# Performance work log

Hardware: AMD Instinct MI355X
Metric: run time of the kernel (lower is better)

The kernel has to match this reference:

```python
import jax, jax.numpy as jnp
import numpy as np

B, N, C = 4, 1024, 512
H = 8
HD = C // H
SCALE = HD ** (-0.5)


def setup_inputs() -> dict:
    key = jax.random.key(0)
    ks = jax.random.split(key, 12)
    s = 0.02
    return {
        "x": jax.random.normal(ks[0], (B, N, C), dtype=jnp.float32),
        "y": jax.random.normal(ks[1], (B, N, C), dtype=jnp.float32),
        "Wqkv1": jax.random.normal(ks[2], (4 * C, C), dtype=jnp.float32) * s,
        "Wqkv2": jax.random.normal(ks[3], (4 * C, C), dtype=jnp.float32) * s,
        "W1": jax.random.normal(ks[4], (C, C), dtype=jnp.float32) * s,
        "b1": jnp.zeros((C,), dtype=jnp.float32),
        "W2": jax.random.normal(ks[5], (C, C), dtype=jnp.float32) * s,
        "b2": jnp.zeros((C,), dtype=jnp.float32),
        "W3": jax.random.normal(ks[6], (C, C), dtype=jnp.float32) * s,
        "b3": jnp.zeros((C,), dtype=jnp.float32),
        "W4": jax.random.normal(ks[7], (C, C), dtype=jnp.float32) * s,
        "b4": jnp.zeros((C,), dtype=jnp.float32),
    }


def _l2norm(t, eps=1e-12):
    # matches F.normalize(dim=-1)
    n = jnp.sqrt(jnp.sum(t * t, axis=-1, keepdims=True))
    return t / jnp.maximum(n, eps)


def _ortho_loss(q, qt):
    # q, qt: [B, H, N, HD]
    qn = _l2norm(q)
    qtn = _l2norm(qt)
    prod = jnp.einsum("bhnd,bhmd->bhnm", qn, qtn)  # [B,H,N,N]
    eye = jnp.eye(N, dtype=prod.dtype)
    off = prod * (1.0 - eye)
    # fro-norm squared of off-diagonal, divided by B*N*N (as in source)
    return jnp.sum(off * off) / (B * N * N)


def _qkv(inp, W):
    # inp: [B,N,C], W: [4C, C] -> [4, B, H, N, HD]
    t = (inp @ W.T).reshape(B, N, 4, H, HD)
    return jnp.transpose(t, (2, 0, 3, 1, 4))


def _attn(q, k, v):
    # q,k,v: [B,H,N,HD] -> [B,N,C]
    scores = jnp.einsum("bhnd,bhmd->bhnm", q, k) * SCALE
    a = jax.nn.softmax(scores, axis=-1)
    o = jnp.einsum("bhnm,bhmd->bhnd", a, v)
    return jnp.transpose(o, (0, 2, 1, 3)).reshape(B, N, C)


def reference(x, y, Wqkv1, Wqkv2, W1, b1, W2, b2, W3, b3, W4, b4):
    qkv1 = _qkv(x, Wqkv1)
    qkv2 = _qkv(y, Wqkv2)
    qx, kx, vx, qtx = qkv1[0], qkv1[1], qkv1[2], qkv1[3]
    qy, ky, vy, qty = qkv2[0], qkv2[1], qkv2[2], qkv2[3]

    lorthx = _ortho_loss(qx, qtx)
    lorthy = _ortho_loss(qy, qty)

    yc = _attn(qx, ky, vy)  # attncy @ vy
    xc = _attn(qy, kx, vx)  # attncx @ vx
    xt = _attn(qtx, kx, vx)
    yt = _attn(qty, ky, vy)

    xc = xc @ W1.T + b1
    yc = yc @ W2.T + b2
    xt = xt @ W3.T + b3
    yt = yt @ W4.T + b4

    # pairwise cosine distance between normalized xc, yc
    xcn = _l2norm(xc)
    ycn = _l2norm(yc)
    cos = jnp.sum(xcn * ycn, axis=-1)
    lc = jnp.mean(1.0 - cos)

    return (xc, yc, xt, yt, lorthx, lorthy, lc)
```

## Files before the change

### kernel.cpp

```cpp
#include <hip/hip_runtime.h>

typedef unsigned short u16;
typedef __attribute__((ext_vector_type(4))) unsigned short u16x4;
typedef __attribute__((ext_vector_type(8))) unsigned short u16x8;
typedef __attribute__((ext_vector_type(4))) float          f32x4;
typedef __attribute__((ext_vector_type(8))) __bf16         bf16x8;

#define MFMA16(a,b,c) __builtin_amdgcn_mfma_f32_16x16x32_bf16((a),(b),(c),0,0,0)
#define SCALE 0.125f
#define SCALE_LOG2E 0.18033688011112042f

__device__ __forceinline__ u16 f2b(float f){
  unsigned u = __builtin_bit_cast(unsigned, f);
  u = (u + 0x7fffu + ((u >> 16) & 1u)) >> 16;
  return (u16)u;
}
__device__ __forceinline__ u16 f2b_trunc(float f){
  return (u16)(__builtin_bit_cast(unsigned, f) >> 16);
}
__device__ __forceinline__ float b2f(u16 v){
  unsigned u = ((unsigned)v) << 16;
  return __builtin_bit_cast(float, u);
}
__device__ __forceinline__ void async16(const u16* g, u16* l){
  __builtin_amdgcn_global_load_lds(
      (const __attribute__((address_space(1))) unsigned*)g,
      (__attribute__((address_space(3))) unsigned*)l, 16, 0, 0);
}
__device__ __forceinline__ int swz(int row, int chunk, int off){
  return row*64 + (((chunk ^ row ^ (row >> 3)) & 7) << 3) + off;
}

__global__ void cast_all_k(const float* __restrict__ x, const float* __restrict__ y,
                           const float* __restrict__ wq1, const float* __restrict__ wq2,
                           const float* __restrict__ w1, const float* __restrict__ w2,
                           const float* __restrict__ w3, const float* __restrict__ w4,
                           u16* __restrict__ dst){
  int i = blockIdx.x * 256 + threadIdx.x;
  const float* s; int base; float sc = 1.f;
  if      (i < 524288)  { s = x;   base = 0;       }
  else if (i < 1048576) { s = y;   base = 524288;  }
  else if (i < 1310720) { s = wq1; base = 1048576;
    int iw = i - base; if (iw < 65536 || iw >= 196608) sc = SCALE_LOG2E; }
  else if (i < 1572864) { s = wq2; base = 1310720;
    int iw = i - base; if (iw < 65536 || iw >= 196608) sc = SCALE_LOG2E; }
  else if (i < 1638400) { s = w1;  base = 1572864; }
  else if (i < 1703936) { s = w2;  base = 1638400; }
  else if (i < 1769472) { s = w3;  base = 1703936; }
  else                  { s = w4;  base = 1769472; }
  float4 v = ((const float4*)s)[i - base];
  u16x4 o; o[0]=f2b(v.x*sc); o[1]=f2b(v.y*sc); o[2]=f2b(v.z*sc); o[3]=f2b(v.w*sc);
  ((u16x4*)dst)[i] = o;
}

__global__ __launch_bounds__(256, 2) void qkv_mega_k(
    const u16* __restrict__ xb, const u16* __restrict__ Wq,
    u16* __restrict__ qkv, u16* __restrict__ vT)
{
  const int i = blockIdx.x;
  const u16 *A, *B; u16* C; int ldc, m0, n0;
  if (i < 512) {
    int z = i >> 8, t = i & 255;
    m0 = (t & 31)*128; n0 = (t >> 5)*128;
    A = xb + (size_t)z*2097152; B = Wq + (size_t)z*1048576;
    C = qkv + (size_t)z*8388608; ldc = 2048;
  } else if (i < 768) {
    int z = (i-512) >> 7, t = (i-512) & 127;
    m0 = (t & 31)*128; n0 = (t >> 5)*128;
    A = xb + (size_t)z*2097152; B = Wq + (size_t)z*1048576 + (size_t)1536*512;
    C = qkv + (size_t)z*8388608 + 1536; ldc = 2048;
  } else {
    int z = (i-768) >> 7, t = (i-768) & 127;
    m0 = (t & 3)*128; n0 = (t >> 2)*128;
    A = Wq + (size_t)z*1048576 + (size_t)1024*512; B = xb + (size_t)z*2097152;
    C = vT + (size_t)z*2097152; ldc = 4096;
  }

  __shared__ u16 As[128*32];
  __shared__ u16 Bs[128*32];
  const int tid  = threadIdx.x;
  const int w    = tid >> 6, lane = tid & 63;
  const int quad = lane >> 4, l16 = lane & 15;
  const int wr   = w >> 1, wc = w & 1;

  f32x4 acc[4][4] = {};
  const int rowa = lane >> 2;
  const int ko   = (lane & 3) * 8;

  for (int k0 = 0; k0 < 512; k0 += 32) {
    __syncthreads();
#pragma unroll
    for (int r = 0; r < 2; ++r) {
      int rb = (r*4 + w) * 16;
      async16(A + (size_t)(m0 + rb + rowa)*512 + k0 + ko, As + (r*4 + w)*512);
      async16(B + (size_t)(n0 + rb + rowa)*512 + k0 + ko, Bs + (r*4 + w)*512);
    }
    __syncthreads();
    bf16x8 af[4], bfr[4];
#pragma unroll
    for (int ii = 0; ii < 4; ++ii)
      af[ii] = *(const bf16x8*)&As[(wr*64 + ii*16 + l16)*32 + quad*8];
#pragma unroll
    for (int j = 0; j < 4; ++j)
      bfr[j] = *(const bf16x8*)&Bs[(wc*64 + j*16 + l16)*32 + quad*8];
#pragma unroll
    for (int ii = 0; ii < 4; ++ii)
#pragma unroll
      for (int j = 0; j < 4; ++j)
        acc[ii][j] = MFMA16(af[ii], bfr[j], acc[ii][j]);
  }
#pragma unroll
  for (int j = 0; j < 4; ++j) {
    int col = n0 + wc*64 + j*16 + l16;
#pragma unroll
    for (int ii = 0; ii < 4; ++ii)
#pragma unroll
      for (int reg = 0; reg < 4; ++reg) {
        int row = m0 + wr*64 + ii*16 + quad*4 + reg;
        C[(size_t)row*ldc + col] = f2b(acc[ii][j][reg]);
      }
  }
}

__global__ __launch_bounds__(256, 2) void gemm_fin_k(
    const u16* __restrict__ A0, size_t aStr, const u16* __restrict__ B0, size_t bStr,
    const float* __restrict__ bias0, const float* __restrict__ bias1,
    const float* __restrict__ bias2, const float* __restrict__ bias3,
    float* __restrict__ C0, size_t cStr)
{
  const int z = blockIdx.z;
  const u16* A = A0 + (size_t)z * aStr;
  const u16* Bm = B0 + (size_t)z * bStr;
  float* Cb = C0 + (size_t)z * cStr;
  const float* bias = (z==0) ? bias0 : (z==1) ? bias1 : (z==2) ? bias2 : bias3;

  __shared__ u16 As[128*32];
  __shared__ u16 Bs[128*32];
  const int tid  = threadIdx.x;
  const int w    = tid >> 6, lane = tid & 63;
  const int quad = lane >> 4, l16 = lane & 15;
  const int wr   = w >> 1, wc = w & 1;
  const int m0 = blockIdx.x * 128, n0 = blockIdx.y * 128;

  f32x4 acc[4][4] = {};
  const int rowa = lane >> 2;
  const int ko   = (lane & 3) * 8;

  for (int k0 = 0; k0 < 512; k0 += 32) {
    __syncthreads();
#pragma unroll
    for (int r = 0; r < 2; ++r) {
      int rb = (r*4 + w) * 16;
      async16(A  + (size_t)(m0 + rb + rowa)*512 + k0 + ko, As + (r*4 + w)*512);
      async16(Bm + (size_t)(n0 + rb + rowa)*512 + k0 + ko, Bs + (r*4 + w)*512);
    }
    __syncthreads();
    bf16x8 af[4], bfr[4];
#pragma unroll
    for (int ii = 0; ii < 4; ++ii)
      af[ii] = *(const bf16x8*)&As[(wr*64 + ii*16 + l16)*32 + quad*8];
#pragma unroll
    for (int j = 0; j < 4; ++j)
      bfr[j] = *(const bf16x8*)&Bs[(wc*64 + j*16 + l16)*32 + quad*8];
#pragma unroll
    for (int ii = 0; ii < 4; ++ii)
#pragma unroll
      for (int j = 0; j < 4; ++j)
        acc[ii][j] = MFMA16(af[ii], bfr[j], acc[ii][j]);
  }
#pragma unroll
  for (int j = 0; j < 4; ++j) {
    int col = n0 + wc*64 + j*16 + l16;
    float bv = bias[col];
#pragma unroll
    for (int ii = 0; ii < 4; ++ii)
#pragma unroll
      for (int reg = 0; reg < 4; ++reg) {
        int row = m0 + wr*64 + ii*16 + quad*4 + reg;
        Cb[(size_t)row*512 + col] = acc[ii][j][reg] + bv;
      }
  }
}

__global__ __launch_bounds__(256, 2) void attn_k(
    const u16* __restrict__ qkv1, const u16* __restrict__ qkv2,
    const u16* __restrict__ vT1, const u16* __restrict__ vT2,
    u16* __restrict__ ao)
{
  const int qt = blockIdx.x, bh = blockIdx.y, p = blockIdx.z;
  const int b = bh >> 3, h = bh & 7;
  const u16* kvsrc = p ? qkv2 : qkv1;
  const u16* vsrc  = p ? vT2 : vT1;
  const u16* qsrcA = p ? qkv1 : qkv2;  const int qoffA = h*64;
  const u16* qsrcB = p ? qkv2 : qkv1;  const int qoffB = 1536 + h*64;
  const int koff = 512 + h*64;
  const size_t tb = (size_t)b * 1024;

  __shared__ u16 Ks[2][4096];
  __shared__ u16 Vt[2][4096];
  __shared__ u16 Ps[4][1024];

  const int tid = threadIdx.x, w = tid >> 6, lane = tid & 63;
  const int quad = lane >> 4, l16 = lane & 15;
  const int srow = tid >> 3, sch = tid & 7;

  u16x8 onesu;
#pragma unroll
  for (int ii = 0; ii < 8; ++ii) onesu[ii] = 0x3f80;
  const bf16x8 ONES = __builtin_bit_cast(bf16x8, onesu);

  bf16x8 qb[2][2][2];
#pragma unroll
  for (int s2 = 0; s2 < 2; ++s2) {
    size_t row = tb + qt*128 + w*32 + s2*16 + l16;
    const u16* qrA = qsrcA + row*2048 + qoffA;
    const u16* qrB = qsrcB + row*2048 + qoffB;
    qb[0][s2][0] = *(const bf16x8*)(qrA + quad*8);
    qb[0][s2][1] = *(const bf16x8*)(qrA + 32 + quad*8);
    qb[1][s2][0] = *(const bf16x8*)(qrB + quad*8);
    qb[1][s2][1] = *(const bf16x8*)(qrB + 32 + quad*8);
  }

  f32x4 oacc[2][2][4] = {};
  f32x4 lacc[2][2] = {};
  u16* myP = Ps[w];

  u16x8 kreg[2], vreg[2];
  auto loadTile = [&](int t){
#pragma unroll
    for (int r = 0; r < 2; ++r) {
      kreg[r] = *(const u16x8*)(kvsrc + (tb + t*64 + r*32 + srow)*2048 + koff + sch*8);
      vreg[r] = *(const u16x8*)(vsrc + (size_t)(h*64 + r*32 + srow)*4096 + tb + t*64 + sch*8);
    }
  };
  auto storeTile = [&](int buf){
#pragma unroll
    for (int r = 0; r < 2; ++r) {
      *(u16x8*)&Ks[buf][swz(r*32 + srow, sch, 0)] = kreg[r];
      *(u16x8*)&Vt[buf][swz(r*32 + srow, sch, 0)] = vreg[r];
    }
  };

  loadTile(0);
  storeTile(0);
  loadTile(1);

  for (int kt = 0; kt < 16; ++kt) {
    const int cur = kt & 1;
    __syncthreads();
    if (kt < 15) storeTile(cur ^ 1);
    if (kt < 14) loadTile(kt + 2);

    bf16x8 ka[4][2], vb[4][2];
#pragma unroll
    for (int j = 0; j < 4; ++j) {
      ka[j][0] = *(const bf16x8*)&Ks[cur][swz(j*16 + l16, quad, 0)];
      ka[j][1] = *(const bf16x8*)&Ks[cur][swz(j*16 + l16, quad + 4, 0)];
      vb[j][0] = *(const bf16x8*)&Vt[cur][swz(j*16 + l16, quad, 0)];
      vb[j][1] = *(const bf16x8*)&Vt[cur][swz(j*16 + l16, quad + 4, 0)];
    }

#pragma unroll
    for (int o = 0; o < 2; ++o)
#pragma unroll
      for (int s2 = 0; s2 < 2; ++s2) {
#pragma unroll
        for (int j = 0; j < 4; ++j) {
          f32x4 t = {};
          __builtin_amdgcn_s_setprio(1);
          t = MFMA16(ka[j][0], qb[o][s2][0], t);
          t = MFMA16(ka[j][1], qb[o][s2][1], t);
          __builtin_amdgcn_s_setprio(0);
          u16x4 pk;
#pragma unroll
          for (int reg = 0; reg < 4; ++reg)
            pk[reg] = f2b_trunc(__builtin_amdgcn_exp2f(t[reg]));
          *(u16x4*)&myP[swz(l16, j*2 + (quad >> 1), (quad & 1)*4)] = pk;
        }
        bf16x8 pa0 = *(const bf16x8*)&myP[swz(l16, quad, 0)];
        bf16x8 pa1 = *(const bf16x8*)&myP[swz(l16, quad + 4, 0)];
        __builtin_amdgcn_s_setprio(1);
#pragma unroll
        for (int j = 0; j < 4; ++j) {
          oacc[o][s2][j] = MFMA16(pa0, vb[j][0], oacc[o][s2][j]);
          oacc[o][s2][j] = MFMA16(pa1, vb[j][1], oacc[o][s2][j]);
        }
        lacc[o][s2] = MFMA16(pa0, ONES, lacc[o][s2]);
        lacc[o][s2] = MFMA16(pa1, ONES, lacc[o][s2]);
        __builtin_amdgcn_s_setprio(0);
      }
  }

#pragma unroll
  for (int o = 0; o < 2; ++o) {
    int a = p + o*2;
    u16* aop = ao + (size_t)a*(4096*512) + (tb + qt*128)*512 + h*64;
#pragma unroll
    for (int s2 = 0; s2 < 2; ++s2) {
#pragma unroll
      for (int reg = 0; reg < 4; ++reg) {
        float linv = 1.f / lacc[o][s2][reg];
        int row = w*32 + s2*16 + quad*4 + reg;
#pragma unroll
        for (int j = 0; j < 4; ++j)
          aop[(size_t)row*512 + j*16 + l16] = f2b(oacc[o][s2][j][reg] * linv);
      }
    }
  }
}

__global__ __launch_bounds__(256, 2) void orthoA_k(
    const u16* __restrict__ qkv1, const u16* __restrict__ qkv2,
    float* __restrict__ Gbuf, float* __restrict__ accum)
{
  const int bh = blockIdx.x, which = blockIdx.y, tg = blockIdx.z;
  const u16* src = which ? qkv2 : qkv1;
  const int b = bh >> 3, h = bh & 7;
  const size_t tb = (size_t)b * 1024;

  __shared__ u16 QnT[4096], QtnT[4096];
  const int tid = threadIdx.x, w = tid >> 6, lane = tid & 63;
  const int quad = lane >> 4, l16 = lane & 15;

  f32x4 gq[4] = {}, gqt[4] = {};
  float diag = 0.f;

  for (int tt = 0; tt < 2; ++tt) {
    int t = tg*2 + tt;
    __syncthreads();
    if (tid < 128) {
      int tok = tid & 63, mat = tid >> 6;
      const u16* pp = src + (tb + t*64 + tok)*2048 + (mat ? 1536 : 0) + h*64;
      u16x8 rowv[8];
#pragma unroll
      for (int i = 0; i < 8; ++i) rowv[i] = *(const u16x8*)(pp + i*8);
      float ss = 0.f;
#pragma unroll
      for (int i = 0; i < 8; ++i)
#pragma unroll
        for (int jj = 0; jj < 8; ++jj) { float f = b2f(rowv[i][jj]); ss += f*f; }
      float inv = 1.f / fmaxf(sqrtf(ss), 1e-12f);
      u16* dst = mat ? QtnT : QnT;
#pragma unroll
      for (int i = 0; i < 8; ++i)
#pragma unroll
        for (int jj = 0; jj < 8; ++jj)
          dst[swz(i*8 + jj, tok >> 3, tok & 7)] = f2b(b2f(rowv[i][jj]) * inv);
      if (mat == 0) {
        const u16* p2 = src + (tb + t*64 + tok)*2048 + 1536 + h*64;
        float ss2 = 0.f, dot = 0.f;
#pragma unroll
        for (int i = 0; i < 8; ++i) {
          u16x8 r2 = *(const u16x8*)(p2 + i*8);
#pragma unroll
          for (int jj = 0; jj < 8; ++jj) {
            float fq = b2f(rowv[i][jj]), ft = b2f(r2[jj]);
            ss2 += ft*ft; dot += fq*ft;
          }
        }
        float inv2 = 1.f / fmaxf(sqrtf(ss2), 1e-12f);
        float dn = dot * inv * inv2;
        diag += dn * dn;
      }
    }
    __syncthreads();
    bf16x8 a0 = *(const bf16x8*)&QnT [swz(w*16 + l16, quad, 0)];
    bf16x8 a1 = *(const bf16x8*)&QnT [swz(w*16 + l16, quad + 4, 0)];
    bf16x8 t0 = *(const bf16x8*)&QtnT[swz(w*16 + l16, quad, 0)];
    bf16x8 t1 = *(const bf16x8*)&QtnT[swz(w*16 + l16, quad + 4, 0)];
#pragma unroll
    for (int j = 0; j < 4; ++j) {
      bf16x8 b0 = *(const bf16x8*)&QnT [swz(j*16 + l16, quad, 0)];
      bf16x8 b1 = *(const bf16x8*)&QnT [swz(j*16 + l16, quad + 4, 0)];
      gq[j]  = MFMA16(a0, b0, gq[j]);
      gq[j]  = MFMA16(a1, b1, gq[j]);
      bf16x8 c0 = *(const bf16x8*)&QtnT[swz(j*16 + l16, quad, 0)];
      bf16x8 c1 = *(const bf16x8*)&QtnT[swz(j*16 + l16, quad + 4, 0)];
      gqt[j] = MFMA16(t0, c0, gqt[j]);
      gqt[j] = MFMA16(t1, c1, gqt[j]);
    }
  }
  float* Gq = Gbuf + (size_t)((which*32 + bh)*2) * 4096;
  float* Gt = Gq + 4096;
#pragma unroll
  for (int j = 0; j < 4; ++j)
#pragma unroll
    for (int reg = 0; reg < 4; ++reg) {
      int row = w*16 + quad*4 + reg, col = j*16 + l16;
      atomicAdd(&Gq[row*64 + col], gq[j][reg]);
      atomicAdd(&Gt[row*64 + col], gqt[j][reg]);
    }
  if (tid < 64) atomicAdd(&accum[which], -diag);
}

__global__ __launch_bounds__(256, 2) void red_k(
    const float* __restrict__ Gbuf, const float* __restrict__ dout,
    float* __restrict__ accum)
{
  const int tid = threadIdx.x;
  if (blockIdx.x < 64) {
    const int w = tid >> 6, lane = tid & 63;
    const int wid = blockIdx.x * 4 + w;
    float acc = 0.f;
    for (int rr = 0; rr < 16; ++rr) {
      int row = wid*16 + rr;
      const float4* xr = (const float4*)(dout + (size_t)row*512 + lane*8);
      const float4* yr = (const float4*)(dout + 2097152 + (size_t)row*512 + lane*8);
      float4 x0 = xr[0], x1 = xr[1], y0 = yr[0], y1 = yr[1];
      float dxy = x0.x*y0.x + x0.y*y0.y + x0.z*y0.z + x0.w*y0.w
                + x1.x*y1.x + x1.y*y1.y + x1.z*y1.z + x1.w*y1.w;
      float sx  = x0.x*x0.x + x0.y*x0.y + x0.z*x0.z + x0.w*x0.w
                + x1.x*x1.x + x1.y*x1.y + x1.z*x1.z + x1.w*x1.w;
      float sy  = y0.x*y0.x + y0.y*y0.y + y0.z*y0.z + y0.w*y0.w
                + y1.x*y1.x + y1.y*y1.y + y1.z*y1.z + y1.w*y1.w;
#pragma unroll
      for (int off = 32; off > 0; off >>= 1) {
        dxy += __shfl_xor(dxy, off);
        sx  += __shfl_xor(sx,  off);
        sy  += __shfl_xor(sy,  off);
      }
      if (lane == 0) {
        float cosv = dxy / (fmaxf(sqrtf(sx), 1e-12f) * fmaxf(sqrtf(sy), 1e-12f));
        acc += 1.f - cosv;
      }
    }
    if (lane == 0) atomicAdd(&accum[2], acc);
  } else {
    const int i = blockIdx.x - 64;
    const int bh = i & 31, which = i >> 5;
    const float* Gq = Gbuf + (size_t)((which*32 + bh)*2) * 4096;
    const float* Gt = Gq + 4096;
    float acc = 0.f;
    for (int idx = tid*4; idx < 4096; idx += 1024) {
      float4 g  = *(const float4*)(Gq + idx);
      float4 gt = *(const float4*)(Gt + idx);
      acc += g.x*gt.x + g.y*gt.y + g.z*gt.z + g.w*gt.w;
    }
    __shared__ float red[256];
    red[tid] = acc; __syncthreads();
    for (int s2 = 128; s2 > 0; s2 >>= 1) {
      if (tid < s2) red[tid] += red[tid + s2];
      __syncthreads();
    }
    if (tid == 0) atomicAdd(&accum[which], red[0]);
  }
}

__global__ void fin_k(const float* __restrict__ accum, float* __restrict__ outs){
  if (threadIdx.x == 0) {
    outs[0] = accum[0] * (1.f/4194304.f);
    outs[1] = accum[1] * (1.f/4194304.f);
    outs[2] = accum[2] * (1.f/4096.f);
  }
}

extern "C" void kernel_launch(void* const* d_in, const int* in_sizes, int n_in,
                              void* d_out, int out_size, void* d_ws, size_t ws_size,
                              hipStream_t stream)
{
  (void)in_sizes; (void)n_in; (void)out_size; (void)ws_size;
  const float* x     = (const float*)d_in[0];
  const float* y     = (const float*)d_in[1];
  const float* Wqkv1 = (const float*)d_in[2];
  const float* Wqkv2 = (const float*)d_in[3];
  const float* W1 = (const float*)d_in[4];
  const float* b1 = (const float*)d_in[5];
  const float* W2 = (const float*)d_in[6];
  const float* b2 = (const float*)d_in[7];
  const float* W3 = (const float*)d_in[8];
  const float* b3 = (const float*)d_in[9];
  const float* W4 = (const float*)d_in[10];
  const float* b4 = (const float*)d_in[11];

  u16* ws   = (u16*)d_ws;
  u16* xb   = ws;
  u16* Wq1b = ws + (size_t)4194304;
  u16* W1b  = ws + (size_t)6291456;
  u16* qkv1 = ws + (size_t)7340032;
  u16* qkv2 = qkv1 + (size_t)8388608;
  u16* aob  = qkv2 + (size_t)8388608;
  float* accum = (float*)(aob + (size_t)8388608);
  float* Gbuf  = accum + 16;
  u16* vT1 = (u16*)d_out;
  u16* vT2 = vT1 + (size_t)2097152;

  hipMemsetAsync(accum, 0, 16, stream);
  hipMemsetAsync(Gbuf, 0, 2097152, stream);

  cast_all_k<<<dim3(7168), dim3(256), 0, stream>>>(x, y, Wqkv1, Wqkv2, W1, W2, W3, W4, xb);

  qkv_mega_k<<<dim3(1024), dim3(256), 0, stream>>>(xb, Wq1b, qkv1, vT1);

  attn_k<<<dim3(8,32,2), 256, 0, stream>>>(qkv1, qkv2, vT1, vT2, aob);

  orthoA_k<<<dim3(32,2,8), 256, 0, stream>>>(qkv1, qkv2, Gbuf, accum);

  float* outb = (float*)d_out;
  gemm_fin_k<<<dim3(32,4,4), 256, 0, stream>>>(
      aob, 2097152, W1b, 262144, b1, b2, b3, b4, outb, 2097152);

  red_k<<<dim3(128), 256, 0, stream>>>(Gbuf, outb, accum);
  fin_k<<<dim3(1), dim3(64), 0, stream>>>(accum, outb + 8388608);
}
```

Baseline: 231.3 us.

## Software-pipeline QK^T/exp with previous PV MFMAs using double-buffered P tiles

Restructures the attention inner loop so each sub-tile's QK^T MFMAs and exp2 conversion overlap with the PV and row-sum MFMAs of the preceding sub-tile. The per-wave P scratch in LDS is doubled to two buffers so one can be written while the other is read. All four score tiles are also computed up front before the exps, which adds independent MFMA work between dependent steps. The cost is extra LDS and higher register pressure from keeping the t[4] tiles and the previous P fragments live, which could hurt occupancy at launch_bounds(256,2).

```diff
diff --git a/kernel.cpp b/kernel.cpp
--- a/kernel.cpp
+++ b/kernel.cpp
@@ -198,7 +198,7 @@
 
   __shared__ u16 Ks[2][4096];
   __shared__ u16 Vt[2][4096];
-  __shared__ u16 Ps[4][1024];
+  __shared__ u16 Ps[4][2][1024];
 
   const int tid = threadIdx.x, w = tid >> 6, lane = tid & 63;
   const int quad = lane >> 4, l16 = lane & 15;
@@ -223,7 +223,6 @@
 
   f32x4 oacc[2][2][4] = {};
   f32x4 lacc[2][2] = {};
-  u16* myP = Ps[w];
 
   u16x8 kreg[2], vreg[2];
   auto loadTile = [&](int t){
@@ -260,35 +259,60 @@
       vb[j][1] = *(const bf16x8*)&Vt[cur][swz(j*16 + l16, quad + 4, 0)];
     }
 
-#pragma unroll
-    for (int o = 0; o < 2; ++o)
-#pragma unroll
-      for (int s2 = 0; s2 < 2; ++s2) {
+    bf16x8 paP0, paP1;
+#pragma unroll
+    for (int idx = 0; idx < 4; ++idx) {
+      const int o = idx >> 1, s2 = idx & 1;
+      u16* wP = Ps[w][idx & 1];
+      f32x4 t[4];
+      __builtin_amdgcn_s_setprio(1);
+#pragma unroll
+      for (int j = 0; j < 4; ++j) {
+        f32x4 z = {};
+        z    = MFMA16(ka[j][0], qb[o][s2][0], z);
+        t[j] = MFMA16(ka[j][1], qb[o][s2][1], z);
+      }
+      __builtin_amdgcn_s_setprio(0);
+      if (idx > 0) {
+        const u16* rP = Ps[w][(idx - 1) & 1];
+        paP0 = *(const bf16x8*)&rP[swz(l16, quad, 0)];
+        paP1 = *(const bf16x8*)&rP[swz(l16, quad + 4, 0)];
+      }
+#pragma unroll
+      for (int j = 0; j < 4; ++j) {
+        u16x4 pk;
+#pragma unroll
+        for (int reg = 0; reg < 4; ++reg)
+          pk[reg] = f2b_trunc(__builtin_amdgcn_exp2f(t[j][reg]));
+        *(u16x4*)&wP[swz(l16, j*2 + (quad >> 1), (quad & 1)*4)] = pk;
+      }
+      if (idx > 0) {
+        const int po = (idx - 1) >> 1, ps2 = (idx - 1) & 1;
+        __builtin_amdgcn_s_setprio(1);
 #pragma unroll
         for (int j = 0; j < 4; ++j) {
-          f32x4 t = {};
-          __builtin_amdgcn_s_setprio(1);
-          t = MFMA16(ka[j][0], qb[o][s2][0], t);
-          t = MFMA16(ka[j][1], qb[o][s2][1], t);
-          __builtin_amdgcn_s_setprio(0);
-          u16x4 pk;
-#pragma unroll
-          for (int reg = 0; reg < 4; ++reg)
-            pk[reg] = f2b_trunc(__builtin_amdgcn_exp2f(t[reg]));
-          *(u16x4*)&myP[swz(l16, j*2 + (quad >> 1), (quad & 1)*4)] = pk;
+          oacc[po][ps2][j] = MFMA16(paP0, vb[j][0], oacc[po][ps2][j]);
+          oacc[po][ps2][j] = MFMA16(paP1, vb[j][1], oacc[po][ps2][j]);
         }
-        bf16x8 pa0 = *(const bf16x8*)&myP[swz(l16, quad, 0)];
-        bf16x8 pa1 = *(const bf16x8*)&myP[swz(l16, quad + 4, 0)];
-        __builtin_amdgcn_s_setprio(1);
-#pragma unroll
-        for (int j = 0; j < 4; ++j) {
-          oacc[o][s2][j] = MFMA16(pa0, vb[j][0], oacc[o][s2][j]);
-          oacc[o][s2][j] = MFMA16(pa1, vb[j][1], oacc[o][s2][j]);
-        }
-        lacc[o][s2] = MFMA16(pa0, ONES, lacc[o][s2]);
-        lacc[o][s2] = MFMA16(pa1, ONES, lacc[o][s2]);
+        lacc[po][ps2] = MFMA16(paP0, ONES, lacc[po][ps2]);
+        lacc[po][ps2] = MFMA16(paP1, ONES, lacc[po][ps2]);
         __builtin_amdgcn_s_setprio(0);
       }
+    }
+    {
+      const u16* rP = Ps[w][1];
+      bf16x8 pa0 = *(const bf16x8*)&rP[swz(l16, quad, 0)];
+      bf16x8 pa1 = *(const bf16x8*)&rP[swz(l16, quad + 4, 0)];
+      __builtin_amdgcn_s_setprio(1);
+#pragma unroll
+      for (int j = 0; j < 4; ++j) {
+        oacc[1][1][j] = MFMA16(pa0, vb[j][0], oacc[1][1][j]);
+        oacc[1][1][j] = MFMA16(pa1, vb[j][1], oacc[1][1][j]);
+      }
+      lacc[1][1] = MFMA16(pa0, ONES, lacc[1][1]);
+      lacc[1][1] = MFMA16(pa1, ONES, lacc[1][1]);
+      __builtin_amdgcn_s_setprio(0);
+    }
   }
 
 #pragma unroll
```

Result: no change. 229.4 us (-0.8%).

## Halve attention query tile, remap blocks per XCD, batch QK MFMAs before softmax

Applied to the files above, without the earlier changes.

The attention kernel now uses a 64-row query tile per block instead of 128, doubling the grid to 1024 blocks and raising launch bounds to 3 blocks per CU. Block indices are remapped so that blocks sharing the same batch/head/pair land on the same XCD, and the QKV GEMM grid is similarly swizzled, both aiming at better L2 reuse of K/V and weights. Inside the loop, all QK^T MFMAs for both query sets are issued together before the exp, and P is staged in a double-sized shared buffer. In exchange, each K/V tile is loaded twice as many times overall, and shared memory per block grows.

```diff
diff --git a/kernel.cpp b/kernel.cpp
--- a/kernel.cpp
+++ b/kernel.cpp
@@ -57,7 +57,7 @@
     const u16* __restrict__ xb, const u16* __restrict__ Wq,
     u16* __restrict__ qkv, u16* __restrict__ vT)
 {
-  const int i = blockIdx.x;
+  const int i = (blockIdx.x & 7) * 128 + (blockIdx.x >> 3);
   const u16 *A, *B; u16* C; int ldc, m0, n0;
   if (i < 512) {
     int z = i >> 8, t = i & 255;
@@ -182,12 +182,16 @@
   }
 }
 
-__global__ __launch_bounds__(256, 2) void attn_k(
+__global__ __launch_bounds__(256, 3) void attn_k(
     const u16* __restrict__ qkv1, const u16* __restrict__ qkv2,
     const u16* __restrict__ vT1, const u16* __restrict__ vT2,
     u16* __restrict__ ao)
 {
-  const int qt = blockIdx.x, bh = blockIdx.y, p = blockIdx.z;
+  const int lin = blockIdx.x;
+  const int xcd = lin & 7, slot = lin >> 3;
+  const int g   = xcd + 8*(slot >> 4);
+  const int qt  = slot & 15;
+  const int bh  = g >> 1, p = g & 1;
   const int b = bh >> 3, h = bh & 7;
   const u16* kvsrc = p ? qkv2 : qkv1;
   const u16* vsrc  = p ? vT2 : vT1;
@@ -198,7 +202,7 @@
 
   __shared__ u16 Ks[2][4096];
   __shared__ u16 Vt[2][4096];
-  __shared__ u16 Ps[4][1024];
+  __shared__ u16 Ps[4][2][1024];
 
   const int tid = threadIdx.x, w = tid >> 6, lane = tid & 63;
   const int quad = lane >> 4, l16 = lane & 15;
@@ -209,21 +213,19 @@
   for (int ii = 0; ii < 8; ++ii) onesu[ii] = 0x3f80;
   const bf16x8 ONES = __builtin_bit_cast(bf16x8, onesu);
 
-  bf16x8 qb[2][2][2];
-#pragma unroll
-  for (int s2 = 0; s2 < 2; ++s2) {
-    size_t row = tb + qt*128 + w*32 + s2*16 + l16;
+  bf16x8 qb[2][2];
+  {
+    size_t row = tb + qt*64 + w*16 + l16;
     const u16* qrA = qsrcA + row*2048 + qoffA;
     const u16* qrB = qsrcB + row*2048 + qoffB;
-    qb[0][s2][0] = *(const bf16x8*)(qrA + quad*8);
-    qb[0][s2][1] = *(const bf16x8*)(qrA + 32 + quad*8);
-    qb[1][s2][0] = *(const bf16x8*)(qrB + quad*8);
-    qb[1][s2][1] = *(const bf16x8*)(qrB + 32 + quad*8);
-  }
-
-  f32x4 oacc[2][2][4] = {};
-  f32x4 lacc[2][2] = {};
-  u16* myP = Ps[w];
+    qb[0][0] = *(const bf16x8*)(qrA + quad*8);
+    qb[0][1] = *(const bf16x8*)(qrA + 32 + quad*8);
+    qb[1][0] = *(const bf16x8*)(qrB + quad*8);
+    qb[1][1] = *(const bf16x8*)(qrB + 32 + quad*8);
+  }
+
+  f32x4 oacc[2][4] = {};
+  f32x4 lacc[2] = {};
 
   u16x8 kreg[2], vreg[2];
   auto loadTile = [&](int t){
@@ -251,60 +253,69 @@
     if (kt < 15) storeTile(cur ^ 1);
     if (kt < 14) loadTile(kt + 2);
 
-    bf16x8 ka[4][2], vb[4][2];
+    bf16x8 ka[4][2];
 #pragma unroll
     for (int j = 0; j < 4; ++j) {
       ka[j][0] = *(const bf16x8*)&Ks[cur][swz(j*16 + l16, quad, 0)];
       ka[j][1] = *(const bf16x8*)&Ks[cur][swz(j*16 + l16, quad + 4, 0)];
+    }
+    f32x4 t[2][4];
+    __builtin_amdgcn_s_setprio(1);
+#pragma unroll
+    for (int o = 0; o < 2; ++o)
+#pragma unroll
+      for (int j = 0; j < 4; ++j) {
+        f32x4 z = {};
+        z       = MFMA16(ka[j][0], qb[o][0], z);
+        t[o][j] = MFMA16(ka[j][1], qb[o][1], z);
+      }
+    __builtin_amdgcn_s_setprio(0);
+#pragma unroll
+    for (int o = 0; o < 2; ++o) {
+      u16* myP = Ps[w][o];
+#pragma unroll
+      for (int j = 0; j < 4; ++j) {
+        u16x4 pk;
+#pragma unroll
+        for (int reg = 0; reg < 4; ++reg)
+          pk[reg] = f2b_trunc(__builtin_amdgcn_exp2f(t[o][j][reg]));
+        *(u16x4*)&myP[swz(l16, j*2 + (quad >> 1), (quad & 1)*4)] = pk;
+      }
+    }
+    bf16x8 vb[4][2];
+#pragma unroll
+    for (int j = 0; j < 4; ++j) {
       vb[j][0] = *(const bf16x8*)&Vt[cur][swz(j*16 + l16, quad, 0)];
       vb[j][1] = *(const bf16x8*)&Vt[cur][swz(j*16 + l16, quad + 4, 0)];
     }
-
-#pragma unroll
-    for (int o = 0; o < 2; ++o)
-#pragma unroll
-      for (int s2 = 0; s2 < 2; ++s2) {
-#pragma unroll
-        for (int j = 0; j < 4; ++j) {
-          f32x4 t = {};
-          __builtin_amdgcn_s_setprio(1);
-          t = MFMA16(ka[j][0], qb[o][s2][0], t);
-          t = MFMA16(ka[j][1], qb[o][s2][1], t);
-          __builtin_amdgcn_s_setprio(0);
-          u16x4 pk;
-#pragma unroll
-          for (int reg = 0; reg < 4; ++reg)
-            pk[reg] = f2b_trunc(__builtin_amdgcn_exp2f(t[reg]));
-          *(u16x4*)&myP[swz(l16, j*2 + (quad >> 1), (quad & 1)*4)] = pk;
-        }
-        bf16x8 pa0 = *(const bf16x8*)&myP[swz(l16, quad, 0)];
-        bf16x8 pa1 = *(const bf16x8*)&myP[swz(l16, quad + 4, 0)];
-        __builtin_amdgcn_s_setprio(1);
-#pragma unroll
-        for (int j = 0; j < 4; ++j) {
-          oacc[o][s2][j] = MFMA16(pa0, vb[j][0], oacc[o][s2][j]);
-          oacc[o][s2][j] = MFMA16(pa1, vb[j][1], oacc[o][s2][j]);
-        }
-        lacc[o][s2] = MFMA16(pa0, ONES, lacc[o][s2]);
-        lacc[o][s2] = MFMA16(pa1, ONES, lacc[o][s2]);
-        __builtin_amdgcn_s_setprio(0);
-      }
+#pragma unroll
+    for (int o = 0; o < 2; ++o) {
+      const u16* rP = Ps[w][o];
+      bf16x8 pa0 = *(const bf16x8*)&rP[swz(l16, quad, 0)];
+      bf16x8 pa1 = *(const bf16x8*)&rP[swz(l16, quad + 4, 0)];
+      __builtin_amdgcn_s_setprio(1);
+#pragma unroll
+      for (int j = 0; j < 4; ++j) {
+        oacc[o][j] = MFMA16(pa0, vb[j][0], oacc[o][j]);
+        oacc[o][j] = MFMA16(pa1, vb[j][1], oacc[o][j]);
+      }
+      lacc[o] = MFMA16(pa0, ONES, lacc[o]);
+      lacc[o] = MFMA16(pa1, ONES, lacc[o]);
+      __builtin_amdgcn_s_setprio(0);
+    }
   }
 
 #pragma unroll
   for (int o = 0; o < 2; ++o) {
     int a = p + o*2;
-    u16* aop = ao + (size_t)a*(4096*512) + (tb + qt*128)*512 + h*64;
-#pragma unroll
-    for (int s2 = 0; s2 < 2; ++s2) {
-#pragma unroll
-      for (int reg = 0; reg < 4; ++reg) {
-        float linv = 1.f / lacc[o][s2][reg];
-        int row = w*32 + s2*16 + quad*4 + reg;
-#pragma unroll
-        for (int j = 0; j < 4; ++j)
-          aop[(size_t)row*512 + j*16 + l16] = f2b(oacc[o][s2][j][reg] * linv);
-      }
+    u16* aop = ao + (size_t)a*(4096*512) + (tb + qt*64)*512 + h*64;
+#pragma unroll
+    for (int reg = 0; reg < 4; ++reg) {
+      float linv = 1.f / lacc[o][reg];
+      int row = w*16 + quad*4 + reg;
+#pragma unroll
+      for (int j = 0; j < 4; ++j)
+        aop[(size_t)row*512 + j*16 + l16] = f2b(oacc[o][j][reg] * linv);
     }
   }
 }
@@ -491,7 +502,7 @@
 
   qkv_mega_k<<<dim3(1024), dim3(256), 0, stream>>>(xb, Wq1b, qkv1, vT1);
 
-  attn_k<<<dim3(8,32,2), 256, 0, stream>>>(qkv1, qkv2, vT1, vT2, aob);
+  attn_k<<<dim3(1024), 256, 0, stream>>>(qkv1, qkv2, vT1, vT2, aob);
 
   orthoA_k<<<dim3(32,2,8), 256, 0, stream>>>(qkv1, qkv2, Gbuf, accum);
 
```

New measurement: 237.8 us. +2.8%, slower.
